# Kernel tuning notes

Measured on AMD Instinct MI355X. Metric: run time of the kernel, lower is better.

## Reference

```python
import jax, jax.numpy as jnp
import numpy as np

N, E, D, G = 100000, 600000, 128, 256  # nodes, edges, feat dim, num graphs
EPS = 1e-5


def graph_norm(x, batch, weight, bias, mean_scale):
    # PyG GraphNorm: per-graph mean/var with learnable mean_scale
    counts = jax.ops.segment_sum(jnp.ones((x.shape[0],), x.dtype), batch, num_segments=G)
    counts = jnp.maximum(counts, 1.0)[:, None]  # [G,1]
    mean = jax.ops.segment_sum(x, batch, num_segments=G) / counts  # [G,D]
    out = x - mean[batch] * mean_scale  # [N,D]
    var = jax.ops.segment_sum(out * out, batch, num_segments=G) / counts  # [G,D]
    inv_std = jax.lax.rsqrt(var + EPS)[batch]  # [N,D]
    return weight * out * inv_std + bias


def sage_conv_max(x, edge_index, w_l, b_l, w_r):
    # SAGEConv(aggr='max'): gather x[src], scatter-max into dst, then two linears
    src, dst = edge_index[0], edge_index[1]
    agg = jax.ops.segment_max(x[src], dst, num_segments=N)  # [N,D], -inf for empty
    agg = jnp.where(jnp.isfinite(agg), agg, 0.0)  # PyG fills empty segments with 0
    return agg @ w_l.T + b_l + x @ w_r.T


def setup_inputs() -> dict:
    key = jax.random.key(0)
    ks = jax.random.split(key, 6)
    x = jax.random.normal(ks[0], (N, D), dtype=jnp.float32)
    edge_index = jax.random.randint(ks[1], (2, E), 0, N, dtype=jnp.int64)
    batch = jnp.sort(jax.random.randint(ks[2], (N,), 0, G, dtype=jnp.int64))
    s = 1.0 / np.sqrt(D)
    return {
        "x": x,
        "edge_index": edge_index,
        "batch": batch,
        "n1_w": jnp.ones((D,), jnp.float32),
        "n1_b": jnp.zeros((D,), jnp.float32),
        "n1_ms": jnp.ones((D,), jnp.float32),
        "n2_w": jnp.ones((D,), jnp.float32),
        "n2_b": jnp.zeros((D,), jnp.float32),
        "n2_ms": jnp.ones((D,), jnp.float32),
        "w_l": jax.random.uniform(ks[3], (D, D), jnp.float32, -s, s),
        "b_l": jax.random.uniform(ks[4], (D,), jnp.float32, -s, s),
        "w_r": jax.random.uniform(ks[5], (D, D), jnp.float32, -s, s),
    }


def reference(x, edge_index, batch, n1_w, n1_b, n1_ms, n2_w, n2_b, n2_ms, w_l, b_l, w_r):
    h = graph_norm(x, batch, n1_w, n1_b, n1_ms)
    h = sage_conv_max(h, edge_index, w_l, b_l, w_r)
    h = jax.nn.relu(x + h)
    h = graph_norm(h, batch, n2_w, n2_b, n2_ms)
    return h
```

## Files before the change

### kernel.cpp

```cpp
#include <hip/hip_runtime.h>
#include <math.h>

#define NN 100000
#define EE 600000
#define DD 128
#define GG 256
#define EPSV 1e-5f

typedef __attribute__((ext_vector_type(8))) __bf16 bf16x8;
typedef __attribute__((ext_vector_type(16))) float f32x16;
typedef __attribute__((ext_vector_type(4))) unsigned short us4;

#define OFF_A1      0
#define OFF_B1      131072
#define OFF_A2      262144
#define OFF_B2      393216
#define OFF_DEG     524288
#define OFF_ROWPTR  924288
#define OFF_CURSOR  1324352
#define OFF_BSUMS   1724352
#define OFF_CNT     1726400
#define OFF_ELIST   1728448
#define OFF_WB      4128448
#define OFF_H1B     4193984
#define WS_NEED_A   (OFF_H1B + 25600000ULL)

#define NB_STATS 782
#define NB_EDGE  2344
#define NB_H1B   12500
#define NB1024   98
#define NT32     3125
#define NB_AGG   12500

__device__ __forceinline__ int lower_bound_i(const int* __restrict__ a, int n, int v) {
    int lo = 0, hi = n;
    while (lo < hi) { int mid = (lo + hi) >> 1; if (a[mid] < v) lo = mid + 1; else hi = mid; }
    return lo;
}

__device__ __forceinline__ unsigned short f2bf(float f) {
    unsigned int u = __float_as_uint(f);
    unsigned int r = u + 0x7fffu + ((u >> 16) & 1u);
    return (unsigned short)(r >> 16);
}

__device__ __forceinline__ void stats_body(
    const float* __restrict__ X, const int* __restrict__ batch,
    float* __restrict__ Sg, float* __restrict__ Qg, int blk)
{
    int t = threadIdx.x;
    int rl = t >> 5, fq = t & 31;
    int r0 = blk * 128;
    int rend = r0 + 128; if (rend > NN) rend = NN;
    __shared__ float ls[8 * 128];
    __shared__ float lq[8 * 128];
    int g0 = batch[r0], g1 = batch[rend - 1];
    const float4* X4 = (const float4*)X;
    for (int g = g0; g <= g1; ++g) {
        int sa = (g == g0) ? r0   : lower_bound_i(batch, NN, g);
        int sb = (g == g1) ? rend : lower_bound_i(batch, NN, g + 1);
        float s0 = 0.f, s1 = 0.f, s2 = 0.f, s3 = 0.f;
        float q0 = 0.f, q1 = 0.f, q2 = 0.f, q3 = 0.f;
        for (int r = sa + rl; r < sb; r += 8) {
            float4 v = X4[r * 32 + fq];
            s0 += v.x; s1 += v.y; s2 += v.z; s3 += v.w;
            q0 += v.x * v.x; q1 += v.y * v.y; q2 += v.z * v.z; q3 += v.w * v.w;
        }
        ls[rl * 128 + fq * 4 + 0] = s0; ls[rl * 128 + fq * 4 + 1] = s1;
        ls[rl * 128 + fq * 4 + 2] = s2; ls[rl * 128 + fq * 4 + 3] = s3;
        lq[rl * 128 + fq * 4 + 0] = q0; lq[rl * 128 + fq * 4 + 1] = q1;
        lq[rl * 128 + fq * 4 + 2] = q2; lq[rl * 128 + fq * 4 + 3] = q3;
        __syncthreads();
        if (t < 32) {
            #pragma unroll
            for (int k = 0; k < 4; k++) {
                float as = 0.f, aq = 0.f;
                #pragma unroll
                for (int j = 0; j < 8; j++) { as += ls[j * 128 + t * 4 + k]; aq += lq[j * 128 + t * 4 + k]; }
                atomicAdd(&Sg[g * DD + t * 4 + k], as);
                atomicAdd(&Qg[g * DD + t * 4 + k], aq);
            }
        }
        __syncthreads();
    }
}

__global__ __launch_bounds__(256) void stats_p1(
    const float* __restrict__ X, const int* __restrict__ batch,
    float* __restrict__ Sg, float* __restrict__ Qg)
{
    stats_body(X, batch, Sg, Qg, blockIdx.x);
}

__global__ __launch_bounds__(256) void statsdeg_kernel(
    const float* __restrict__ X, const int* __restrict__ batch,
    float* __restrict__ Sg, float* __restrict__ Qg,
    const int* __restrict__ dst, int* __restrict__ deg)
{
    int b = blockIdx.x;
    if (b < NB_STATS) { stats_body(X, batch, Sg, Qg, b); return; }
    int e = (b - NB_STATS) * 256 + threadIdx.x;
    if (e < EE) atomicAdd(&deg[dst[e]], 1);
}

__global__ __launch_bounds__(128) void finalize_kernel(
    const int* __restrict__ batch, float* S, float* Q,
    const float* __restrict__ w, const float* __restrict__ bb, const float* __restrict__ ms,
    unsigned short* __restrict__ wb, const float* __restrict__ wl, const float* __restrict__ wr,
    int* __restrict__ cnt, int doW)
{
    int g = blockIdx.x;
    if (g >= GG) {
        if (!doW) return;
        const float* W = (g == GG) ? wl : wr;
        int kofs = (g == GG) ? 0 : 128;
        for (int tt = threadIdx.x; tt < DD * 32; tt += 128) {
            int j = tt >> 5, k4 = tt & 31;
            float4 v = ((const float4*)W)[j * 32 + k4];
            us4 o = { f2bf(v.x), f2bf(v.y), f2bf(v.z), f2bf(v.w) };
            *(us4*)&wb[j * 256 + kofs + k4 * 4] = o;
        }
        return;
    }
    __shared__ int sh[2];
    if (threadIdx.x == 0) { sh[0] = lower_bound_i(batch, NN, g); sh[1] = lower_bound_i(batch, NN, g + 1); }
    __syncthreads();
    int c_n = sh[1] - sh[0];
    if (cnt && threadIdx.x == 0) cnt[g] = c_n;
    float c = (float)(c_n > 0 ? c_n : 1);
    float inv_c = 1.0f / c;
    int d = threadIdx.x;
    float m  = S[g * DD + d] * inv_c;
    float qm = Q[g * DD + d] * inv_c;
    float sc = ms[d];
    float var = qm - m * m * sc * (2.0f - sc);
    float Ad = w[d] * rsqrtf(var + EPSV);
    S[g * DD + d] = Ad;
    Q[g * DD + d] = bb[d] - Ad * m * sc;
}

__global__ __launch_bounds__(256) void h1bscan_kernel(
    const float* __restrict__ X, const int* __restrict__ batch,
    const float* __restrict__ A1, const float* __restrict__ B1, unsigned short* __restrict__ h1b,
    const int* __restrict__ deg, int* __restrict__ bsums)
{
    int blk = blockIdx.x;
    if (blk < NB_H1B) {
        int f = blk * 256 + threadIdx.x;
        int i = f >> 5, c = f & 31;
        int g = batch[i];
        float4 v = ((const float4*)X)[f];
        float4 a = ((const float4*)A1)[g * 32 + c];
        float4 b = ((const float4*)B1)[g * 32 + c];
        us4 o = { f2bf(fmaf(a.x, v.x, b.x)), f2bf(fmaf(a.y, v.y, b.y)),
                  f2bf(fmaf(a.z, v.z, b.z)), f2bf(fmaf(a.w, v.w, b.w)) };
        *(us4*)&h1b[i * DD + c * 4] = o;
        return;
    }
    int b = blk - NB_H1B, t = threadIdx.x;
    int base = b * 1024 + t * 4;
    int v = 0;
    #pragma unroll
    for (int k = 0; k < 4; k++) { int i = base + k; if (i < NN) v += deg[i]; }
    __shared__ int sd[256];
    sd[t] = v; __syncthreads();
    for (int off = 128; off > 0; off >>= 1) { if (t < off) sd[t] += sd[t + off]; __syncthreads(); }
    if (t == 0) bsums[b] = sd[0];
}

__global__ __launch_bounds__(256) void scan1(const int* __restrict__ deg, int* __restrict__ bsums) {
    int b = blockIdx.x, t = threadIdx.x;
    int base = b * 1024 + t * 4;
    int v = 0;
    #pragma unroll
    for (int k = 0; k < 4; k++) { int i = base + k; if (i < NN) v += deg[i]; }
    __shared__ int sd[256];
    sd[t] = v; __syncthreads();
    for (int off = 128; off > 0; off >>= 1) { if (t < off) sd[t] += sd[t + off]; __syncthreads(); }
    if (t == 0) bsums[b] = sd[0];
}

__global__ __launch_bounds__(256) void scan3(const int* __restrict__ deg, const int* __restrict__ bsums,
                                             int* __restrict__ rowptr, int* __restrict__ cursor) {
    int b = blockIdx.x, t = threadIdx.x;
    int boff = 0;
    for (int j = 0; j < b; j++) boff += bsums[j];
    int base = b * 1024 + t * 4;
    int d0 = 0, d1 = 0, d2 = 0, d3 = 0;
    if (base     < NN) d0 = deg[base];
    if (base + 1 < NN) d1 = deg[base + 1];
    if (base + 2 < NN) d2 = deg[base + 2];
    if (base + 3 < NN) d3 = deg[base + 3];
    int tsum = d0 + d1 + d2 + d3;
    __shared__ int sd[256];
    sd[t] = tsum; __syncthreads();
    for (int off = 1; off < 256; off <<= 1) {
        int a = (t >= off) ? sd[t - off] : 0;
        __syncthreads();
        sd[t] += a;
        __syncthreads();
    }
    int exc = sd[t] - tsum + boff;
    int p0 = exc, p1 = exc + d0, p2 = exc + d0 + d1, p3 = exc + d0 + d1 + d2;
    if (base     < NN) { rowptr[base]     = p0; cursor[base]     = p0; }
    if (base + 1 < NN) { rowptr[base + 1] = p1; cursor[base + 1] = p1; }
    if (base + 2 < NN) { rowptr[base + 2] = p2; cursor[base + 2] = p2; }
    if (base + 3 < NN) { rowptr[base + 3] = p3; cursor[base + 3] = p3; }
    if (b == 0 && t == 0) rowptr[NN] = EE;
}

__global__ __launch_bounds__(256) void fill_kernel(const int* __restrict__ src, const int* __restrict__ dst,
                                                   int* __restrict__ cursor, int* __restrict__ elist) {
    int e = blockIdx.x * 256 + threadIdx.x;
    if (e < EE) {
        int p = atomicAdd(&cursor[dst[e]], 1);
        elist[p] = src[e];
    }
}

__global__ __launch_bounds__(256) void aggmax_kernel(
    const unsigned short* __restrict__ h1b,
    const int* __restrict__ rowptr, const int* __restrict__ elist,
    unsigned short* __restrict__ aggb)
{
    int hw = threadIdx.x >> 5;
    int j  = threadIdx.x & 31;
    int i  = blockIdx.x * 8 + hw;
    int beg = rowptr[i], end = rowptr[i + 1];
    float a0 = -INFINITY, a1 = -INFINITY, a2 = -INFINITY, a3 = -INFINITY;
    int last = end - 1;
    for (int e = beg; e < end; e += 8) {
        int n[8];
        #pragma unroll
        for (int k = 0; k < 8; k++) { int t2 = e + k; n[k] = elist[t2 < last ? t2 : last]; }
        us4 p[8];
        #pragma unroll
        for (int k = 0; k < 8; k++) p[k] = *(const us4*)(h1b + (size_t)n[k] * DD + j * 4);
        #pragma unroll
        for (int k = 0; k < 8; k++) {
            a0 = fmaxf(a0, __uint_as_float((unsigned)p[k][0] << 16));
            a1 = fmaxf(a1, __uint_as_float((unsigned)p[k][1] << 16));
            a2 = fmaxf(a2, __uint_as_float((unsigned)p[k][2] << 16));
            a3 = fmaxf(a3, __uint_as_float((unsigned)p[k][3] << 16));
        }
    }
    us4 r4 = { 0, 0, 0, 0 };
    if (end > beg) {
        r4[0] = (unsigned short)(__float_as_uint(a0) >> 16);
        r4[1] = (unsigned short)(__float_as_uint(a1) >> 16);
        r4[2] = (unsigned short)(__float_as_uint(a2) >> 16);
        r4[3] = (unsigned short)(__float_as_uint(a3) >> 16);
    }
    *(us4*)&aggb[(size_t)i * 256 + j * 4] = r4;
}

#define USTR 264
__global__ __launch_bounds__(256) void gemm_mega(
    const float* __restrict__ X, const unsigned short* __restrict__ h1b,
    const int* __restrict__ batch,
    const unsigned short* __restrict__ wb, const float* __restrict__ blv,
    float* __restrict__ Sg2, float* __restrict__ Qg2, float* __restrict__ out)
{
    __shared__ unsigned short sU[32 * USTR];
    __shared__ int sBatch[32];
    int tid = threadIdx.x;
    int i0 = blockIdx.x * 32;
    int lane = tid & 63, wave = tid >> 6;
    int m = lane & 31, hf = lane >> 5;
    const unsigned short* aggb = (const unsigned short*)out;

    for (int t = tid; t < 32 * 32; t += 256) {
        int r = t >> 5, c = t & 31;
        int i = i0 + r;
        uint4 v;
        if (c < 16) {
            v = ((const uint4*)(aggb + (size_t)i * 256))[c];
            *(uint4*)&sU[r * USTR + c * 8] = v;
        } else {
            v = ((const uint4*)(h1b + (size_t)i * DD))[c - 16];
            *(uint4*)&sU[r * USTR + 128 + (c - 16) * 8] = v;
        }
    }
    if (tid < 32) sBatch[tid] = batch[i0 + tid];
    __syncthreads();

    int col = wave * 32 + m;
    const unsigned short* bcol = wb + col * 256 + hf * 8;
    const unsigned short* arow = &sU[m * USTR + hf * 8];

    f32x16 acc;
    #pragma unroll
    for (int r = 0; r < 16; r++) acc[r] = 0.f;
    #pragma unroll
    for (int s = 0; s < 16; s++) {
        bf16x8 b = *(const bf16x8*)(bcol + s * 16);
        bf16x8 a = *(const bf16x8*)(arow + s * 16);
        acc = __builtin_amdgcn_mfma_f32_32x32x16_bf16(a, b, acc, 0, 0, 0);
    }

    float blc = blv[col];
    float s_run = 0.f, q_run = 0.f;
    int cur_g = -1;
    #pragma unroll
    for (int reg = 0; reg < 16; reg++) {
        int rl = (reg & 3) + 8 * (reg >> 2) + 4 * hf;
        int i = i0 + rl;
        float v = X[i * DD + col] + blc + acc[reg];
        v = v > 0.f ? v : 0.f;
        out[i * DD + col] = v;
        int g = sBatch[rl];
        if (g != cur_g) {
            if (cur_g >= 0) {
                atomicAdd(&Sg2[cur_g * DD + col], s_run);
                atomicAdd(&Qg2[cur_g * DD + col], q_run);
            }
            cur_g = g; s_run = 0.f; q_run = 0.f;
        }
        s_run += v; q_run += v * v;
    }
    if (cur_g >= 0) {
        atomicAdd(&Sg2[cur_g * DD + col], s_run);
        atomicAdd(&Qg2[cur_g * DD + col], q_run);
    }
}

__global__ __launch_bounds__(256) void apply_a(
    float* __restrict__ H, const int* __restrict__ batch,
    const float* __restrict__ Sg2, const float* __restrict__ Qg2, const int* __restrict__ cnt,
    const float* __restrict__ w2, const float* __restrict__ b2, const float* __restrict__ ms2)
{
    int f = blockIdx.x * 256 + threadIdx.x;
    if (f >= NN * 32) return;
    int i = f >> 5, c = f & 31;
    int g = batch[i];
    int cg = cnt[g];
    float invc = 1.0f / (float)(cg > 0 ? cg : 1);
    float4 S  = ((const float4*)Sg2)[g * 32 + c];
    float4 Q  = ((const float4*)Qg2)[g * 32 + c];
    float4 W  = ((const float4*)w2)[c];
    float4 Bv = ((const float4*)b2)[c];
    float4 Ms = ((const float4*)ms2)[c];
    float4 v = ((float4*)H)[f];
    {
        float mm = S.x * invc, qm = Q.x * invc;
        float A = W.x * rsqrtf(qm - mm * mm * Ms.x * (2.0f - Ms.x) + EPSV);
        v.x = fmaf(A, v.x, Bv.x - A * mm * Ms.x);
    }
    {
        float mm = S.y * invc, qm = Q.y * invc;
        float A = W.y * rsqrtf(qm - mm * mm * Ms.y * (2.0f - Ms.y) + EPSV);
        v.y = fmaf(A, v.y, Bv.y - A * mm * Ms.y);
    }
    {
        float mm = S.z * invc, qm = Q.z * invc;
        float A = W.z * rsqrtf(qm - mm * mm * Ms.z * (2.0f - Ms.z) + EPSV);
        v.z = fmaf(A, v.z, Bv.z - A * mm * Ms.z);
    }
    {
        float mm = S.w * invc, qm = Q.w * invc;
        float A = W.w * rsqrtf(qm - mm * mm * Ms.w * (2.0f - Ms.w) + EPSV);
        v.w = fmaf(A, v.w, Bv.w - A * mm * Ms.w);
    }
    ((float4*)H)[f] = v;
}

__global__ __launch_bounds__(256) void apply_b(float* __restrict__ H, const int* __restrict__ batch,
                                               const float* __restrict__ A2, const float* __restrict__ B2) {
    int f = blockIdx.x * 256 + threadIdx.x;
    if (f >= NN * 32) return;
    int i = f >> 5, c = f & 31;
    int g = batch[i];
    float4 v = ((float4*)H)[f];
    float4 a = ((const float4*)A2)[g * 32 + c];
    float4 b = ((const float4*)B2)[g * 32 + c];
    v.x = fmaf(a.x, v.x, b.x); v.y = fmaf(a.y, v.y, b.y);
    v.z = fmaf(a.z, v.z, b.z); v.w = fmaf(a.w, v.w, b.w);
    ((float4*)H)[f] = v;
}

__global__ __launch_bounds__(256) void agg_b(
    const float* __restrict__ X, const int* __restrict__ batch,
    const float* __restrict__ A1, const float* __restrict__ B1,
    const int* __restrict__ rowptr, const int* __restrict__ elist, float* __restrict__ H)
{
    int i = blockIdx.x * 2 + (threadIdx.x >> 7);
    int d = threadIdx.x & 127;
    int beg = rowptr[i], end = rowptr[i + 1];
    float acc = -INFINITY;
    int e = beg;
    for (; e + 2 <= end; e += 2) {
        int s0 = elist[e], s1 = elist[e + 1];
        int g0 = batch[s0], g1 = batch[s1];
        float v0 = fmaf(A1[g0 * DD + d], X[s0 * DD + d], B1[g0 * DD + d]);
        float v1 = fmaf(A1[g1 * DD + d], X[s1 * DD + d], B1[g1 * DD + d]);
        acc = fmaxf(acc, fmaxf(v0, v1));
    }
    for (; e < end; e++) {
        int s = elist[e]; int g = batch[s];
        acc = fmaxf(acc, fmaf(A1[g * DD + d], X[s * DD + d], B1[g * DD + d]));
    }
    if (end == beg) acc = 0.f;
    H[i * DD + d] = acc;
}

#define BM 128
#define LDT 72
__global__ __launch_bounds__(256) void gemm_b(
    const float* __restrict__ X, const int* __restrict__ batch,
    const float* __restrict__ A1, const float* __restrict__ B1,
    const float* __restrict__ wl, const float* __restrict__ blv, const float* __restrict__ wr,
    float* __restrict__ H)
{
    __shared__ unsigned short Ut[BM * LDT];
    __shared__ unsigned short Wt[DD * LDT];
    int i0 = blockIdx.x * BM;
    int tid = threadIdx.x;
    int lane = tid & 63, wave = tid >> 6;
    int wrow = (wave >> 1) * 64, wcol = (wave & 1) * 64;
    int m = lane & 31, hf = lane >> 5;

    f32x16 acc00, acc01, acc10, acc11;
    #pragma unroll
    for (int r = 0; r < 16; r++) { acc00[r] = 0.f; acc01[r] = 0.f; acc10[r] = 0.f; acc11[r] = 0.f; }

    for (int c = 0; c < 4; c++) {
        __syncthreads();
        for (int t = tid; t < BM * 16; t += 256) {
            int r = t >> 4, c4 = t & 15;
            int i = i0 + r; if (i >= NN) i = NN - 1;
            float4 v;
            if (c < 2) {
                v = ((const float4*)H)[i * 32 + c * 16 + c4];
            } else {
                int g = batch[i];
                float4 xv = ((const float4*)X)[i * 32 + (c - 2) * 16 + c4];
                float4 a = ((const float4*)A1)[g * 32 + (c - 2) * 16 + c4];
                float4 b = ((const float4*)B1)[g * 32 + (c - 2) * 16 + c4];
                v.x = fmaf(a.x, xv.x, b.x); v.y = fmaf(a.y, xv.y, b.y);
                v.z = fmaf(a.z, xv.z, b.z); v.w = fmaf(a.w, xv.w, b.w);
            }
            us4 o = { f2bf(v.x), f2bf(v.y), f2bf(v.z), f2bf(v.w) };
            *(us4*)&Ut[r * LDT + c4 * 4] = o;
        }
        {
            const float* Wsrc = (c < 2) ? wl : wr;
            int kb = (c & 1) * 16;
            for (int t = tid; t < DD * 16; t += 256) {
                int j = t >> 4, c4 = t & 15;
                float4 v = ((const float4*)Wsrc)[j * 32 + kb + c4];
                us4 o = { f2bf(v.x), f2bf(v.y), f2bf(v.z), f2bf(v.w) };
                *(us4*)&Wt[j * LDT + c4 * 4] = o;
            }
        }
        __syncthreads();
        #pragma unroll
        for (int kk = 0; kk < 4; kk++) {
            int kb2 = kk * 16 + hf * 8;
            bf16x8 a0 = *(const bf16x8*)&Ut[(wrow      + m) * LDT + kb2];
            bf16x8 a1 = *(const bf16x8*)&Ut[(wrow + 32 + m) * LDT + kb2];
            bf16x8 b0 = *(const bf16x8*)&Wt[(wcol      + m) * LDT + kb2];
            bf16x8 b1 = *(const bf16x8*)&Wt[(wcol + 32 + m) * LDT + kb2];
            acc00 = __builtin_amdgcn_mfma_f32_32x32x16_bf16(a0, b0, acc00, 0, 0, 0);
            acc01 = __builtin_amdgcn_mfma_f32_32x32x16_bf16(a0, b1, acc01, 0, 0, 0);
            acc10 = __builtin_amdgcn_mfma_f32_32x32x16_bf16(a1, b0, acc10, 0, 0, 0);
            acc11 = __builtin_amdgcn_mfma_f32_32x32x16_bf16(a1, b1, acc11, 0, 0, 0);
        }
    }

    int col0 = wcol + m, col1 = wcol + 32 + m;
    float bl0 = blv[col0], bl1 = blv[col1];
    #pragma unroll
    for (int reg = 0; reg < 16; reg++) {
        int rl = (reg & 3) + 8 * (reg >> 2) + 4 * hf;
        int ia = i0 + wrow + rl;
        int ib = i0 + wrow + 32 + rl;
        if (ia < NN) {
            float v0 = X[ia * DD + col0] + bl0 + acc00[reg];
            float v1 = X[ia * DD + col1] + bl1 + acc01[reg];
            H[ia * DD + col0] = v0 > 0.f ? v0 : 0.f;
            H[ia * DD + col1] = v1 > 0.f ? v1 : 0.f;
        }
        if (ib < NN) {
            float v0 = X[ib * DD + col0] + bl0 + acc10[reg];
            float v1 = X[ib * DD + col1] + bl1 + acc11[reg];
            H[ib * DD + col0] = v0 > 0.f ? v0 : 0.f;
            H[ib * DD + col1] = v1 > 0.f ? v1 : 0.f;
        }
    }
}

extern "C" void kernel_launch(void* const* d_in, const int* in_sizes, int n_in,
                              void* d_out, int out_size, void* d_ws, size_t ws_size,
                              hipStream_t stream) {
    const float* x    = (const float*)d_in[0];
    const int*   ei   = (const int*)d_in[1];
    const int*   batch= (const int*)d_in[2];
    const float* n1w  = (const float*)d_in[3];
    const float* n1b  = (const float*)d_in[4];
    const float* n1ms = (const float*)d_in[5];
    const float* n2w  = (const float*)d_in[6];
    const float* n2b  = (const float*)d_in[7];
    const float* n2ms = (const float*)d_in[8];
    const float* wl   = (const float*)d_in[9];
    const float* bl   = (const float*)d_in[10];
    const float* wr   = (const float*)d_in[11];
    float* out = (float*)d_out;

    char* w = (char*)d_ws;
    float* A1     = (float*)(w + OFF_A1);
    float* B1     = (float*)(w + OFF_B1);
    float* A2     = (float*)(w + OFF_A2);
    float* B2     = (float*)(w + OFF_B2);
    int*   deg    = (int*)(w + OFF_DEG);
    int*   rowptr = (int*)(w + OFF_ROWPTR);
    int*   cursor = (int*)(w + OFF_CURSOR);
    int*   bsums  = (int*)(w + OFF_BSUMS);
    int*   cnt    = (int*)(w + OFF_CNT);
    int*   elist  = (int*)(w + OFF_ELIST);
    unsigned short* wb  = (unsigned short*)(w + OFF_WB);
    unsigned short* h1b = (unsigned short*)(w + OFF_H1B);

    const int* src = ei;
    const int* dst = ei + EE;
    bool bigws = (ws_size >= WS_NEED_A);

    hipMemsetAsync(w, 0, OFF_ROWPTR, stream);

    statsdeg_kernel<<<NB_STATS + NB_EDGE, 256, 0, stream>>>(x, batch, A1, B1, dst, deg);
    finalize_kernel<<<GG + 2, 128, 0, stream>>>(batch, A1, B1, n1w, n1b, n1ms,
                                                wb, wl, wr, cnt, bigws ? 1 : 0);

    if (bigws) {
        h1bscan_kernel<<<NB_H1B + NB1024, 256, 0, stream>>>(x, batch, A1, B1, h1b, deg, bsums);
        scan3<<<NB1024, 256, 0, stream>>>(deg, bsums, rowptr, cursor);
        fill_kernel<<<NB_EDGE, 256, 0, stream>>>(src, dst, cursor, elist);

        aggmax_kernel<<<NB_AGG, 256, 0, stream>>>(h1b, rowptr, elist, (unsigned short*)out);

        gemm_mega<<<NT32, 256, 0, stream>>>(x, h1b, batch, wb, bl, A2, B2, out);

        apply_a<<<NB_H1B, 256, 0, stream>>>(out, batch, A2, B2, cnt, n2w, n2b, n2ms);
    } else {
        scan1<<<NB1024, 256, 0, stream>>>(deg, bsums);
        scan3<<<NB1024, 256, 0, stream>>>(deg, bsums, rowptr, cursor);
        fill_kernel<<<NB_EDGE, 256, 0, stream>>>(src, dst, cursor, elist);

        agg_b<<<NN / 2, 256, 0, stream>>>(x, batch, A1, B1, rowptr, elist, out);
        gemm_b<<<(NN + BM - 1) / BM, 256, 0, stream>>>(x, batch, A1, B1, wl, bl, wr, out);

        stats_p1<<<NB_STATS, 256, 0, stream>>>(out, batch, A2, B2);
        finalize_kernel<<<GG, 128, 0, stream>>>(batch, A2, B2, n2w, n2b, n2ms,
                                                (unsigned short*)nullptr,
                                                (const float*)nullptr, (const float*)nullptr,
                                                (int*)nullptr, 0);
        apply_b<<<NB_H1B, 256, 0, stream>>>(out, batch, A2, B2);
    }
}
```

Before: 304.4 us.

## Fuse per-graph norm1 stats, finalize and bf16 normalize into one front kernel

Replaces the stats/atomics, finalize and h1b-normalize kernels on the fast path with one kernel that uses one 512-thread block per graph. Each block computes its graph's sum and sum of squares, derives scale and shift in shared memory, then rereads its rows and writes normalized bf16 features. The same launch also carries the degree counting and the weight bf16 conversion. This removes two launches, the float atomics for norm1 stats and part of the memset, at the cost of a separate scan1 launch and load imbalance from ~390-row graphs handled by a single block each.

After: 299.7 us. About the same (-1.5%).

```diff
diff --git a/kernel.cpp b/kernel.cpp
--- a/kernel.cpp
+++ b/kernel.cpp
@@ -11,18 +11,19 @@
 typedef __attribute__((ext_vector_type(16))) float f32x16;
 typedef __attribute__((ext_vector_type(4))) unsigned short us4;
 
-#define OFF_A1      0
-#define OFF_B1      131072
-#define OFF_A2      262144
-#define OFF_B2      393216
-#define OFF_DEG     524288
+#define OFF_A2      0
+#define OFF_B2      131072
+#define OFF_DEG     262144
+#define MEMSET_A    662144
+#define OFF_A1      662144
+#define OFF_B1      793216
 #define OFF_ROWPTR  924288
-#define OFF_CURSOR  1324352
-#define OFF_BSUMS   1724352
-#define OFF_CNT     1726400
-#define OFF_ELIST   1728448
-#define OFF_WB      4128448
-#define OFF_H1B     4193984
+#define OFF_CURSOR  1324296
+#define OFF_BSUMS   1724296
+#define OFF_CNT     1724688
+#define OFF_ELIST   1725712
+#define OFF_WB      4125712
+#define OFF_H1B     4191248
 #define WS_NEED_A   (OFF_H1B + 25600000ULL)
 
 #define NB_STATS 782
@@ -32,6 +33,10 @@
 #define NT32     3125
 #define NB_AGG   12500
 
+#define FB_GRAPH 256
+#define FB_EDGE  1172
+#define FB_WB    2
+
 __device__ __forceinline__ int lower_bound_i(const int* __restrict__ a, int n, int v) {
     int lo = 0, hi = n;
     while (lo < hi) { int mid = (lo + hi) >> 1; if (a[mid] < v) lo = mid + 1; else hi = mid; }
@@ -44,128 +49,81 @@
     return (unsigned short)(r >> 16);
 }
 
-__device__ __forceinline__ void stats_body(
+__global__ __launch_bounds__(512) void fused_front(
     const float* __restrict__ X, const int* __restrict__ batch,
-    float* __restrict__ Sg, float* __restrict__ Qg, int blk)
-{
-    int t = threadIdx.x;
-    int rl = t >> 5, fq = t & 31;
-    int r0 = blk * 128;
-    int rend = r0 + 128; if (rend > NN) rend = NN;
-    __shared__ float ls[8 * 128];
-    __shared__ float lq[8 * 128];
-    int g0 = batch[r0], g1 = batch[rend - 1];
+    const float* __restrict__ n1w, const float* __restrict__ n1bv, const float* __restrict__ n1ms,
+    const float* __restrict__ wl, const float* __restrict__ wr,
+    const int* __restrict__ dst, int* __restrict__ deg, int* __restrict__ cnt,
+    unsigned short* __restrict__ wb, unsigned short* __restrict__ h1b)
+{
+    int b = blockIdx.x, tid = threadIdx.x;
+    if (b >= FB_GRAPH) {
+        int bb = b - FB_GRAPH;
+        if (bb < FB_EDGE) {
+            int e = bb * 512 + tid;
+            if (e < EE) atomicAdd(&deg[dst[e]], 1);
+        } else {
+            int wsel = bb - FB_EDGE;
+            const float* W = wsel ? wr : wl;
+            int kofs = wsel ? 128 : 0;
+            for (int tt = tid; tt < DD * 32; tt += 512) {
+                int j = tt >> 5, k4 = tt & 31;
+                float4 v = ((const float4*)W)[j * 32 + k4];
+                us4 o = { f2bf(v.x), f2bf(v.y), f2bf(v.z), f2bf(v.w) };
+                *(us4*)&wb[j * 256 + kofs + k4 * 4] = o;
+            }
+        }
+        return;
+    }
+    int g = b;
+    __shared__ int sh[2];
+    __shared__ float ls[16 * 128];
+    __shared__ float lq[16 * 128];
+    __shared__ __align__(16) float sA[128];
+    __shared__ __align__(16) float sB[128];
+    if (tid == 0) { sh[0] = lower_bound_i(batch, NN, g); sh[1] = lower_bound_i(batch, NN, g + 1); }
+    __syncthreads();
+    int r0 = sh[0], r1 = sh[1];
+    int c_n = r1 - r0;
+    if (tid == 0) cnt[g] = c_n;
+    int rl = tid >> 5, fq = tid & 31;
+    float s0 = 0.f, s1 = 0.f, s2 = 0.f, s3 = 0.f;
+    float q0 = 0.f, q1 = 0.f, q2 = 0.f, q3 = 0.f;
     const float4* X4 = (const float4*)X;
-    for (int g = g0; g <= g1; ++g) {
-        int sa = (g == g0) ? r0   : lower_bound_i(batch, NN, g);
-        int sb = (g == g1) ? rend : lower_bound_i(batch, NN, g + 1);
-        float s0 = 0.f, s1 = 0.f, s2 = 0.f, s3 = 0.f;
-        float q0 = 0.f, q1 = 0.f, q2 = 0.f, q3 = 0.f;
-        for (int r = sa + rl; r < sb; r += 8) {
-            float4 v = X4[r * 32 + fq];
-            s0 += v.x; s1 += v.y; s2 += v.z; s3 += v.w;
-            q0 += v.x * v.x; q1 += v.y * v.y; q2 += v.z * v.z; q3 += v.w * v.w;
-        }
-        ls[rl * 128 + fq * 4 + 0] = s0; ls[rl * 128 + fq * 4 + 1] = s1;
-        ls[rl * 128 + fq * 4 + 2] = s2; ls[rl * 128 + fq * 4 + 3] = s3;
-        lq[rl * 128 + fq * 4 + 0] = q0; lq[rl * 128 + fq * 4 + 1] = q1;
-        lq[rl * 128 + fq * 4 + 2] = q2; lq[rl * 128 + fq * 4 + 3] = q3;
-        __syncthreads();
-        if (t < 32) {
-            #pragma unroll
-            for (int k = 0; k < 4; k++) {
-                float as = 0.f, aq = 0.f;
-                #pragma unroll
-                for (int j = 0; j < 8; j++) { as += ls[j * 128 + t * 4 + k]; aq += lq[j * 128 + t * 4 + k]; }
-                atomicAdd(&Sg[g * DD + t * 4 + k], as);
-                atomicAdd(&Qg[g * DD + t * 4 + k], aq);
-            }
-        }
-        __syncthreads();
-    }
-}
-
-__global__ __launch_bounds__(256) void stats_p1(
-    const float* __restrict__ X, const int* __restrict__ batch,
-    float* __restrict__ Sg, float* __restrict__ Qg)
-{
-    stats_body(X, batch, Sg, Qg, blockIdx.x);
-}
-
-__global__ __launch_bounds__(256) void statsdeg_kernel(
-    const float* __restrict__ X, const int* __restrict__ batch,
-    float* __restrict__ Sg, float* __restrict__ Qg,
-    const int* __restrict__ dst, int* __restrict__ deg)
-{
-    int b = blockIdx.x;
-    if (b < NB_STATS) { stats_body(X, batch, Sg, Qg, b); return; }
-    int e = (b - NB_STATS) * 256 + threadIdx.x;
-    if (e < EE) atomicAdd(&deg[dst[e]], 1);
-}
-
-__global__ __launch_bounds__(128) void finalize_kernel(
-    const int* __restrict__ batch, float* S, float* Q,
-    const float* __restrict__ w, const float* __restrict__ bb, const float* __restrict__ ms,
-    unsigned short* __restrict__ wb, const float* __restrict__ wl, const float* __restrict__ wr,
-    int* __restrict__ cnt, int doW)
-{
-    int g = blockIdx.x;
-    if (g >= GG) {
-        if (!doW) return;
-        const float* W = (g == GG) ? wl : wr;
-        int kofs = (g == GG) ? 0 : 128;
-        for (int tt = threadIdx.x; tt < DD * 32; tt += 128) {
-            int j = tt >> 5, k4 = tt & 31;
-            float4 v = ((const float4*)W)[j * 32 + k4];
-            us4 o = { f2bf(v.x), f2bf(v.y), f2bf(v.z), f2bf(v.w) };
-            *(us4*)&wb[j * 256 + kofs + k4 * 4] = o;
-        }
-        return;
-    }
-    __shared__ int sh[2];
-    if (threadIdx.x == 0) { sh[0] = lower_bound_i(batch, NN, g); sh[1] = lower_bound_i(batch, NN, g + 1); }
+    for (int r = r0 + rl; r < r1; r += 16) {
+        float4 v = X4[r * 32 + fq];
+        s0 += v.x; s1 += v.y; s2 += v.z; s3 += v.w;
+        q0 += v.x * v.x; q1 += v.y * v.y; q2 += v.z * v.z; q3 += v.w * v.w;
+    }
+    ls[rl * 128 + fq * 4 + 0] = s0; ls[rl * 128 + fq * 4 + 1] = s1;
+    ls[rl * 128 + fq * 4 + 2] = s2; ls[rl * 128 + fq * 4 + 3] = s3;
+    lq[rl * 128 + fq * 4 + 0] = q0; lq[rl * 128 + fq * 4 + 1] = q1;
+    lq[rl * 128 + fq * 4 + 2] = q2; lq[rl * 128 + fq * 4 + 3] = q3;
     __syncthreads();
-    int c_n = sh[1] - sh[0];
-    if (cnt && threadIdx.x == 0) cnt[g] = c_n;
-    float c = (float)(c_n > 0 ? c_n : 1);
-    float inv_c = 1.0f / c;
-    int d = threadIdx.x;
-    float m  = S[g * DD + d] * inv_c;
-    float qm = Q[g * DD + d] * inv_c;
-    float sc = ms[d];
-    float var = qm - m * m * sc * (2.0f - sc);
-    float Ad = w[d] * rsqrtf(var + EPSV);
-    S[g * DD + d] = Ad;
-    Q[g * DD + d] = bb[d] - Ad * m * sc;
-}
-
-__global__ __launch_bounds__(256) void h1bscan_kernel(
-    const float* __restrict__ X, const int* __restrict__ batch,
-    const float* __restrict__ A1, const float* __restrict__ B1, unsigned short* __restrict__ h1b,
-    const int* __restrict__ deg, int* __restrict__ bsums)
-{
-    int blk = blockIdx.x;
-    if (blk < NB_H1B) {
-        int f = blk * 256 + threadIdx.x;
-        int i = f >> 5, c = f & 31;
-        int g = batch[i];
-        float4 v = ((const float4*)X)[f];
-        float4 a = ((const float4*)A1)[g * 32 + c];
-        float4 b = ((const float4*)B1)[g * 32 + c];
-        us4 o = { f2bf(fmaf(a.x, v.x, b.x)), f2bf(fmaf(a.y, v.y, b.y)),
-                  f2bf(fmaf(a.z, v.z, b.z)), f2bf(fmaf(a.w, v.w, b.w)) };
-        *(us4*)&h1b[i * DD + c * 4] = o;
-        return;
-    }
-    int b = blk - NB_H1B, t = threadIdx.x;
-    int base = b * 1024 + t * 4;
-    int v = 0;
-    #pragma unroll
-    for (int k = 0; k < 4; k++) { int i = base + k; if (i < NN) v += deg[i]; }
-    __shared__ int sd[256];
-    sd[t] = v; __syncthreads();
-    for (int off = 128; off > 0; off >>= 1) { if (t < off) sd[t] += sd[t + off]; __syncthreads(); }
-    if (t == 0) bsums[b] = sd[0];
+    if (tid < 128) {
+        int d = tid;
+        float as = 0.f, aq = 0.f;
+        #pragma unroll
+        for (int j = 0; j < 16; j++) { as += ls[j * 128 + d]; aq += lq[j * 128 + d]; }
+        float c = (float)(c_n > 0 ? c_n : 1);
+        float inv_c = 1.0f / c;
+        float m  = as * inv_c;
+        float qm = aq * inv_c;
+        float sc = n1ms[d];
+        float var = qm - m * m * sc * (2.0f - sc);
+        float Ad = n1w[d] * rsqrtf(var + EPSV);
+        sA[d] = Ad;
+        sB[d] = n1bv[d] - Ad * m * sc;
+    }
+    __syncthreads();
+    for (int r = r0 + rl; r < r1; r += 16) {
+        float4 v = X4[r * 32 + fq];
+        float4 a = ((const float4*)sA)[fq];
+        float4 bb2 = ((const float4*)sB)[fq];
+        us4 o = { f2bf(fmaf(a.x, v.x, bb2.x)), f2bf(fmaf(a.y, v.y, bb2.y)),
+                  f2bf(fmaf(a.z, v.z, bb2.z)), f2bf(fmaf(a.w, v.w, bb2.w)) };
+        *(us4*)&h1b[r * DD + fq * 4] = o;
+    }
 }
 
 __global__ __launch_bounds__(256) void scan1(const int* __restrict__ deg, int* __restrict__ bsums) {
@@ -272,12 +230,11 @@
     for (int t = tid; t < 32 * 32; t += 256) {
         int r = t >> 5, c = t & 31;
         int i = i0 + r;
-        uint4 v;
         if (c < 16) {
-            v = ((const uint4*)(aggb + (size_t)i * 256))[c];
+            uint4 v = ((const uint4*)(aggb + (size_t)i * 256))[c];
             *(uint4*)&sU[r * USTR + c * 8] = v;
         } else {
-            v = ((const uint4*)(h1b + (size_t)i * DD))[c - 16];
+            uint4 v = ((const uint4*)(h1b + (size_t)i * DD))[c - 16];
             *(uint4*)&sU[r * USTR + 128 + (c - 16) * 8] = v;
         }
     }
@@ -333,8 +290,8 @@
     if (f >= NN * 32) return;
     int i = f >> 5, c = f & 31;
     int g = batch[i];
-    int cg = cnt[g];
-    float invc = 1.0f / (float)(cg > 0 ? cg : 1);
+    int cg_ = cnt[g];
+    float invc = 1.0f / (float)(cg_ > 0 ? cg_ : 1);
     float4 S  = ((const float4*)Sg2)[g * 32 + c];
     float4 Q  = ((const float4*)Qg2)[g * 32 + c];
     float4 W  = ((const float4*)w2)[c];
@@ -362,6 +319,92 @@
         v.w = fmaf(A, v.w, Bv.w - A * mm * Ms.w);
     }
     ((float4*)H)[f] = v;
+}
+
+
+__device__ __forceinline__ void stats_body(
+    const float* __restrict__ X, const int* __restrict__ batch,
+    float* __restrict__ Sg, float* __restrict__ Qg, int blk,
+    float* __restrict__ ls, float* __restrict__ lq)
+{
+    int t = threadIdx.x;
+    int rl = t >> 5, fq = t & 31;
+    int r0 = blk * 128;
+    int rend = r0 + 128; if (rend > NN) rend = NN;
+    int g0 = batch[r0], g1 = batch[rend - 1];
+    const float4* X4 = (const float4*)X;
+    for (int g = g0; g <= g1; ++g) {
+        int sa = (g == g0) ? r0   : lower_bound_i(batch, NN, g);
+        int sb = (g == g1) ? rend : lower_bound_i(batch, NN, g + 1);
+        float s0 = 0.f, s1 = 0.f, s2 = 0.f, s3 = 0.f;
+        float q0 = 0.f, q1 = 0.f, q2 = 0.f, q3 = 0.f;
+        for (int r = sa + rl; r < sb; r += 8) {
+            float4 v = X4[r * 32 + fq];
+            s0 += v.x; s1 += v.y; s2 += v.z; s3 += v.w;
+            q0 += v.x * v.x; q1 += v.y * v.y; q2 += v.z * v.z; q3 += v.w * v.w;
+        }
+        ls[rl * 128 + fq * 4 + 0] = s0; ls[rl * 128 + fq * 4 + 1] = s1;
+        ls[rl * 128 + fq * 4 + 2] = s2; ls[rl * 128 + fq * 4 + 3] = s3;
+        lq[rl * 128 + fq * 4 + 0] = q0; lq[rl * 128 + fq * 4 + 1] = q1;
+        lq[rl * 128 + fq * 4 + 2] = q2; lq[rl * 128 + fq * 4 + 3] = q3;
+        __syncthreads();
+        if (t < 32) {
+            #pragma unroll
+            for (int k = 0; k < 4; k++) {
+                float as = 0.f, aq = 0.f;
+                #pragma unroll
+                for (int j = 0; j < 8; j++) { as += ls[j * 128 + t * 4 + k]; aq += lq[j * 128 + t * 4 + k]; }
+                atomicAdd(&Sg[g * DD + t * 4 + k], as);
+                atomicAdd(&Qg[g * DD + t * 4 + k], aq);
+            }
+        }
+        __syncthreads();
+    }
+}
+
+__global__ __launch_bounds__(256) void stats_p1(
+    const float* __restrict__ X, const int* __restrict__ batch,
+    float* __restrict__ Sg, float* __restrict__ Qg)
+{
+    __shared__ float ls[8 * 128];
+    __shared__ float lq[8 * 128];
+    stats_body(X, batch, Sg, Qg, blockIdx.x, ls, lq);
+}
+
+__global__ __launch_bounds__(256) void statsdeg_kernel(
+    const float* __restrict__ X, const int* __restrict__ batch,
+    float* __restrict__ Sg, float* __restrict__ Qg,
+    const int* __restrict__ dst, int* __restrict__ deg)
+{
+    __shared__ float ls[8 * 128];
+    __shared__ float lq[8 * 128];
+    int b = blockIdx.x;
+    if (b < NB_STATS) { stats_body(X, batch, Sg, Qg, b, ls, lq); return; }
+    int e = (b - NB_STATS) * 256 + threadIdx.x;
+    if (e < EE) atomicAdd(&deg[dst[e]], 1);
+}
+
+__global__ __launch_bounds__(128) void finalize_kernel(
+    const int* __restrict__ batch, float* S, float* Q,
+    const float* __restrict__ w, const float* __restrict__ bb, const float* __restrict__ ms,
+    int* __restrict__ cnt)
+{
+    int g = blockIdx.x;
+    __shared__ int sh[2];
+    if (threadIdx.x == 0) { sh[0] = lower_bound_i(batch, NN, g); sh[1] = lower_bound_i(batch, NN, g + 1); }
+    __syncthreads();
+    int c_n = sh[1] - sh[0];
+    if (cnt && threadIdx.x == 0) cnt[g] = c_n;
+    float c = (float)(c_n > 0 ? c_n : 1);
+    float inv_c = 1.0f / c;
+    int d = threadIdx.x;
+    float m  = S[g * DD + d] * inv_c;
+    float qm = Q[g * DD + d] * inv_c;
+    float sc = ms[d];
+    float var = qm - m * m * sc * (2.0f - sc);
+    float Ad = w[d] * rsqrtf(var + EPSV);
+    S[g * DD + d] = Ad;
+    Q[g * DD + d] = bb[d] - Ad * m * sc;
 }
 
 __global__ __launch_bounds__(256) void apply_b(float* __restrict__ H, const int* __restrict__ batch,
@@ -507,11 +550,11 @@
     float* out = (float*)d_out;
 
     char* w = (char*)d_ws;
-    float* A1     = (float*)(w + OFF_A1);
-    float* B1     = (float*)(w + OFF_B1);
     float* A2     = (float*)(w + OFF_A2);
     float* B2     = (float*)(w + OFF_B2);
     int*   deg    = (int*)(w + OFF_DEG);
+    float* A1     = (float*)(w + OFF_A1);
+    float* B1     = (float*)(w + OFF_B1);
     int*   rowptr = (int*)(w + OFF_ROWPTR);
     int*   cursor = (int*)(w + OFF_CURSOR);
     int*   bsums  = (int*)(w + OFF_BSUMS);
@@ -524,35 +567,36 @@
     const int* dst = ei + EE;
     bool bigws = (ws_size >= WS_NEED_A);
 
-    hipMemsetAsync(w, 0, OFF_ROWPTR, stream);
-
-    statsdeg_kernel<<<NB_STATS + NB_EDGE, 256, 0, stream>>>(x, batch, A1, B1, dst, deg);
-    finalize_kernel<<<GG + 2, 128, 0, stream>>>(batch, A1, B1, n1w, n1b, n1ms,
-                                                wb, wl, wr, cnt, bigws ? 1 : 0);
-
     if (bigws) {
-        h1bscan_kernel<<<NB_H1B + NB1024, 256, 0, stream>>>(x, batch, A1, B1, h1b, deg, bsums);
-        scan3<<<NB1024, 256, 0, stream>>>(deg, bsums, rowptr, cursor);
-        fill_kernel<<<NB_EDGE, 256, 0, stream>>>(src, dst, cursor, elist);
-
-        aggmax_kernel<<<NB_AGG, 256, 0, stream>>>(h1b, rowptr, elist, (unsigned short*)out);
-
-        gemm_mega<<<NT32, 256, 0, stream>>>(x, h1b, batch, wb, bl, A2, B2, out);
-
-        apply_a<<<NB_H1B, 256, 0, stream>>>(out, batch, A2, B2, cnt, n2w, n2b, n2ms);
-    } else {
+        hipMemsetAsync(w, 0, MEMSET_A, stream);
+
+        fused_front<<<FB_GRAPH + FB_EDGE + FB_WB, 512, 0, stream>>>(
+            x, batch, n1w, n1b, n1ms, wl, wr, dst, deg, cnt, wb, h1b);
+
         scan1<<<NB1024, 256, 0, stream>>>(deg, bsums);
         scan3<<<NB1024, 256, 0, stream>>>(deg, bsums, rowptr, cursor);
         fill_kernel<<<NB_EDGE, 256, 0, stream>>>(src, dst, cursor, elist);
 
+        aggmax_kernel<<<NB_AGG, 256, 0, stream>>>(h1b, rowptr, elist, (unsigned short*)out);
+
+        gemm_mega<<<NT32, 256, 0, stream>>>(x, h1b, batch, wb, bl, A2, B2, out);
+
+        apply_a<<<NB_H1B, 256, 0, stream>>>(out, batch, A2, B2, cnt, n2w, n2b, n2ms);
+    } else {
+        hipMemsetAsync(w, 0, OFF_ROWPTR, stream);
+
+        statsdeg_kernel<<<NB_STATS + NB_EDGE, 256, 0, stream>>>(x, batch, A1, B1, dst, deg);
+        finalize_kernel<<<GG, 128, 0, stream>>>(batch, A1, B1, n1w, n1b, n1ms, cnt);
+
+        scan1<<<NB1024, 256, 0, stream>>>(deg, bsums);
+        scan3<<<NB1024, 256, 0, stream>>>(deg, bsums, rowptr, cursor);
+        fill_kernel<<<NB_EDGE, 256, 0, stream>>>(src, dst, cursor, elist);
+
         agg_b<<<NN / 2, 256, 0, stream>>>(x, batch, A1, B1, rowptr, elist, out);
         gemm_b<<<(NN + BM - 1) / BM, 256, 0, stream>>>(x, batch, A1, B1, wl, bl, wr, out);
 
         stats_p1<<<NB_STATS, 256, 0, stream>>>(out, batch, A2, B2);
-        finalize_kernel<<<GG, 128, 0, stream>>>(batch, A2, B2, n2w, n2b, n2ms,
-                                                (unsigned short*)nullptr,
-                                                (const float*)nullptr, (const float*)nullptr,
-                                                (int*)nullptr, 0);
+        finalize_kernel<<<GG, 128, 0, stream>>>(batch, A2, B2, n2w, n2b, n2ms, (int*)nullptr);
         apply_b<<<NB_H1B, 256, 0, stream>>>(out, batch, A2, B2);
     }
 }
```
